# Optimization experiments

Measured on AMD Instinct MI355X. Metric: run time of the kernel, lower is better.

Reference implementation:

```python
import jax, jax.numpy as jnp
import numpy as np

N_NODES = 100000
BN_EPS = 1e-5


def gcn_conv(x, W, b, src, dst, n_nodes):
    # PyG GCNConv: linear transform, add self loops, symmetric deg^-1/2 normalization, sum-aggregate to dst, add bias
    h = x @ W.T  # [N, out_dim]
    loops = jnp.arange(n_nodes, dtype=src.dtype)
    src_a = jnp.concatenate([src, loops])
    dst_a = jnp.concatenate([dst, loops])
    deg = jnp.zeros((n_nodes,), dtype=h.dtype).at[dst_a].add(1.0)  # includes self loops, so deg >= 1
    dinv = jax.lax.rsqrt(deg)
    norm = dinv[src_a] * dinv[dst_a]  # [E+N]
    msgs = h[src_a] * norm[:, None]  # gather + scale
    out = jax.ops.segment_sum(msgs, dst_a, num_segments=n_nodes)
    return out + b


def batch_norm(x, gamma, beta):
    # BatchNorm1d in training mode: per-feature batch mean/var (biased)
    mean = jnp.mean(x, axis=0)
    var = jnp.var(x, axis=0)
    return (x - mean) * jax.lax.rsqrt(var + BN_EPS) * gamma + beta


def setup_inputs() -> dict:
    key = jax.random.key(0)
    ks = jax.random.split(key, 8)
    n, e = N_NODES, 1600000
    d_in, d_hid, d_out = 128, 128, 64
    x = jax.random.normal(ks[0], (n, d_in), dtype=jnp.float32)
    edge_index = jax.random.randint(ks[1], (2, e), 0, n, dtype=jnp.int64)
    W1 = jax.random.normal(ks[2], (d_hid, d_in), dtype=jnp.float32) / np.sqrt(d_in)
    b1 = jnp.zeros((d_hid,), dtype=jnp.float32)
    gamma = jnp.ones((d_hid,), dtype=jnp.float32)
    beta = jnp.zeros((d_hid,), dtype=jnp.float32)
    W2 = jax.random.normal(ks[3], (d_out, d_hid), dtype=jnp.float32) / np.sqrt(d_hid)
    b2 = jnp.zeros((d_out,), dtype=jnp.float32)
    return {"x": x, "edge_index": edge_index, "W1": W1, "b1": b1,
            "gamma": gamma, "beta": beta, "W2": W2, "b2": b2}


def reference(x, edge_index, W1, b1, gamma, beta, W2, b2):
    src, dst = edge_index[0], edge_index[1]
    n = x.shape[0]
    h = gcn_conv(x, W1, b1, src, dst, n)          # layer 0 conv
    h = batch_norm(h, gamma, beta)                 # BN
    h = jax.nn.relu(h)                             # ReLU (dropout p=0 -> identity)
    out = gcn_conv(h, W2, b2, src, dst, n)         # layer 1 conv (no BN/act on last layer)
    return out
```

## Files before the change

### kernel.cpp

```cpp
#include <hip/hip_runtime.h>

constexpr float BN_EPS = 1e-5f;
#define BSH 7
#define NBMAX 1024

typedef __attribute__((ext_vector_type(8))) short bf16x8;
typedef __attribute__((ext_vector_type(4))) float f32x4;

__device__ inline float2 bf2x2(unsigned int v) {
    union { unsigned int i; float f; } a, b;
    a.i = v << 16;
    b.i = v & 0xFFFF0000u;
    return make_float2(a.f, b.f);
}
__device__ inline float bf2f(unsigned short u) {
    union { unsigned int i; float f; } a;
    a.i = ((unsigned int)u) << 16;
    return a.f;
}
__device__ inline unsigned short f2bf(float f) {
    union { float f; unsigned int i; } c;
    c.f = f;
    unsigned int i = c.i;
    return (unsigned short)((i + 0x7FFFu + ((i >> 16) & 1u)) >> 16);
}

__device__ inline int wsw(int row, int k) {
    return row * 128 + ((((k >> 3) ^ (row & 7)) << 3) | (k & 7));
}

__global__ void k_zero(int* __restrict__ gcount) {
    gcount[threadIdx.x] = 0;
}

__global__ __launch_bounds__(256) void k_hist(const int* __restrict__ dst, int* __restrict__ gcount,
                                              int E, int NB) {
    __shared__ int lh[NBMAX];
    const int tid = threadIdx.x;
    for (int i = tid; i < NBMAX; i += 256) lh[i] = 0;
    __syncthreads();
    const int base = blockIdx.x * 8192;
#pragma unroll
    for (int i = 0; i < 32; ++i) {
        int e = base + i * 256 + tid;
        if (e < E) atomicAdd(&lh[dst[e] >> BSH], 1);
    }
    __syncthreads();
    for (int b = tid; b < NB; b += 256) {
        int c = lh[b];
        if (c) atomicAdd(&gcount[b], c);
    }
}

__global__ __launch_bounds__(1024) void k_scanb(const int* __restrict__ gcount, int* __restrict__ gstart,
                                                int* __restrict__ cursor, float* __restrict__ stats, int NB) {
    __shared__ int tmp[1024];
    const int t = threadIdx.x;
    int v = (t < NB) ? gcount[t] : 0;
    tmp[t] = v;
    __syncthreads();
    for (int off = 1; off < 1024; off <<= 1) {
        int u = (t >= off) ? tmp[t - off] : 0;
        __syncthreads();
        tmp[t] += u;
        __syncthreads();
    }
    if (t < NB) { int ex = tmp[t] - v; gstart[t] = ex; cursor[t] = ex; }
    if (t == NB - 1) gstart[NB] = tmp[t];
    if (t < 512) stats[t] = 0.f;
}

__global__ __launch_bounds__(256) void k_scatter(const int* __restrict__ src, const int* __restrict__ dst,
                                                 int* __restrict__ cursor, int2* __restrict__ pairs,
                                                 int E, int NB) {
    __shared__ int lh[NBMAX], lbase[NBMAX], gbase[NBMAX], lcur[NBMAX];
    __shared__ int2 buf[4096];
    __shared__ unsigned short bo[4096];
    const int tid = threadIdx.x;
    for (int i = tid; i < NBMAX; i += 256) lh[i] = 0;
    __syncthreads();
    const int base = blockIdx.x * 4096;
    const int cnt = min(4096, E - base);
#pragma unroll
    for (int i = 0; i < 16; ++i) {
        int e = base + i * 256 + tid;
        if (e < E) atomicAdd(&lh[dst[e] >> BSH], 1);
    }
    __syncthreads();
    int s0 = lh[tid * 4], s1 = lh[tid * 4 + 1], s2 = lh[tid * 4 + 2], s3 = lh[tid * 4 + 3];
    int ts = s0 + s1 + s2 + s3;
    lcur[tid] = ts;
    __syncthreads();
    for (int off = 1; off < 256; off <<= 1) {
        int u = (tid >= off) ? lcur[tid - off] : 0;
        __syncthreads();
        lcur[tid] += u;
        __syncthreads();
    }
    int ex = lcur[tid] - ts;
    lbase[tid * 4] = ex;
    lbase[tid * 4 + 1] = ex + s0;
    lbase[tid * 4 + 2] = ex + s0 + s1;
    lbase[tid * 4 + 3] = ex + s0 + s1 + s2;
    __syncthreads();
    for (int b = tid; b < NB; b += 256) {
        int c = lh[b];
        gbase[b] = c ? atomicAdd(&cursor[b], c) : 0;
    }
    for (int i = tid; i < NBMAX; i += 256) lcur[i] = 0;
    __syncthreads();
#pragma unroll
    for (int i = 0; i < 16; ++i) {
        int e = base + i * 256 + tid;
        if (e < E) {
            int d = dst[e];
            int b = d >> BSH;
            int p = lbase[b] + atomicAdd(&lcur[b], 1);
            buf[p] = make_int2(src[e], d);
            bo[p] = (unsigned short)b;
        }
    }
    __syncthreads();
#pragma unroll
    for (int i = 0; i < 16; ++i) {
        int p = i * 256 + tid;
        if (p < cnt) {
            int b = bo[p];
            pairs[gbase[b] + (p - lbase[b])] = buf[p];
        }
    }
}

__global__ __launch_bounds__(256) void k_build(const int2* __restrict__ pairs, const int* __restrict__ gstart,
                                               int* __restrict__ rowptr, int* __restrict__ rowend,
                                               float* __restrict__ dinv, int* __restrict__ esrc, int n) {
    __shared__ int lh[128], lsc[128], lcur[128];
    const int tid = threadIdx.x;
    const int b = blockIdx.x;
    const int e0 = gstart[b], e1 = gstart[b + 1];
    const int node0 = b << BSH;
    if (tid < 128) lh[tid] = 0;
    __syncthreads();
    for (int e = e0 + tid; e < e1; e += 256) atomicAdd(&lh[pairs[e].y - node0], 1);
    __syncthreads();
    int v = (tid < 128) ? lh[tid] : 0;
    if (tid < 128) lsc[tid] = v;
    __syncthreads();
    for (int off = 1; off < 128; off <<= 1) {
        int u = (tid >= off && tid < 128) ? lsc[tid - off] : 0;
        __syncthreads();
        if (tid < 128) lsc[tid] += u;
        __syncthreads();
    }
    if (tid < 128) {
        int ex = lsc[tid] - v;
        lcur[tid] = ex;
        int node = node0 + tid;
        if (node < n) {
            int rp = e0 + ex;
            rowptr[node] = rp;
            rowend[node] = rp + v;
            dinv[node] = rsqrtf((float)(v + 1));
        }
    }
    __syncthreads();
    for (int e = e0 + tid; e < e1; e += 256) {
        int2 p = pairs[e];
        int pos = atomicAdd(&lcur[p.y - node0], 1);
        esrc[e0 + pos] = p.x;
    }
}

__global__ __launch_bounds__(256) void k_gemm1(const float* __restrict__ x,
                                               const float* __restrict__ W1,
                                               const float* __restrict__ dinv,
                                               unsigned short* __restrict__ g1, int n) {
    __shared__ unsigned short Ws[128 * 128];
    const int tid = threadIdx.x;
#pragma unroll
    for (int i = 0; i < 16; ++i) {
        int idx4 = i * 256 + tid;
        int j = idx4 >> 5;
        int k = (idx4 & 31) * 4;
        float4 v = *(const float4*)&W1[(size_t)j * 128 + k];
        ushort4 u;
        u.x = f2bf(v.x); u.y = f2bf(v.y); u.z = f2bf(v.z); u.w = f2bf(v.w);
        *(ushort2*)&Ws[wsw(j, k)] = make_ushort2(u.x, u.y);
        *(ushort2*)&Ws[wsw(j, k + 2)] = make_ushort2(u.z, u.w);
    }
    __syncthreads();
    const int wave = tid >> 6, l = tid & 63;
    const int am = l & 15;
    const int kg = l >> 4;
    const int row0 = blockIdx.x * 64 + wave * 16;
    const int grow = row0 + am;
    const float* xrow = &x[(size_t)(grow < n ? grow : 0) * 128];
    f32x4 acc[8] = {};
#pragma unroll
    for (int k0 = 0; k0 < 128; k0 += 32) {
        const int kk = k0 + kg * 8;
        float4 a0 = *(const float4*)&xrow[kk];
        float4 a1 = *(const float4*)&xrow[kk + 4];
        union { unsigned short u[8]; bf16x8 v; } af;
        af.u[0] = f2bf(a0.x); af.u[1] = f2bf(a0.y); af.u[2] = f2bf(a0.z); af.u[3] = f2bf(a0.w);
        af.u[4] = f2bf(a1.x); af.u[5] = f2bf(a1.y); af.u[6] = f2bf(a1.z); af.u[7] = f2bf(a1.w);
#pragma unroll
        for (int ct = 0; ct < 8; ++ct) {
            union { uint4 q; bf16x8 v; } bf;
            bf.q = *(const uint4*)&Ws[wsw(ct * 16 + am, kk)];
            acc[ct] = __builtin_amdgcn_mfma_f32_16x16x32_bf16(af.v, bf.v, acc[ct], 0, 0, 0);
        }
    }
#pragma unroll
    for (int r = 0; r < 4; ++r) {
        int orow = row0 + kg * 4 + r;
        if (orow < n) {
            float di = dinv[orow];
#pragma unroll
            for (int ct = 0; ct < 8; ++ct)
                g1[(size_t)orow * 128 + ct * 16 + am] = f2bf(acc[ct][r] * di);
        }
    }
}

__global__ __launch_bounds__(256) void k_pull1(const int* __restrict__ rowptr, const int* __restrict__ rowend,
                                               const int* __restrict__ esrc, const unsigned short* __restrict__ g,
                                               const float* __restrict__ dinv, const float* __restrict__ b1,
                                               unsigned short* __restrict__ h1, float* __restrict__ stats, int n) {
    __shared__ float2 sSum[4][64];
    __shared__ float2 sSq[4][64];
    const int wid = threadIdx.x >> 6, lane = threadIdx.x & 63;
    const int gw = blockIdx.x * 4 + wid;
    const int nw = gridDim.x * 4;
    const float2 bias = *(const float2*)&b1[lane * 2];
    float2 psum = {0.f, 0.f}, psq = {0.f, 0.f};
    for (int node = gw; node < n; node += nw) {
        const int b = rowptr[node], e = rowend[node];
        float2 a0 = bf2x2(*(const unsigned int*)&g[(size_t)node * 128 + lane * 2]);
        float2 a1 = {0.f, 0.f}, a2 = {0.f, 0.f}, a3 = {0.f, 0.f};
        float2 a4 = {0.f, 0.f}, a5 = {0.f, 0.f}, a6 = {0.f, 0.f}, a7 = {0.f, 0.f};
        int j = b;
        for (; j + 8 <= e; j += 8) {
            int s0 = esrc[j + 0], s1 = esrc[j + 1], s2 = esrc[j + 2], s3 = esrc[j + 3];
            int s4 = esrc[j + 4], s5 = esrc[j + 5], s6 = esrc[j + 6], s7 = esrc[j + 7];
            unsigned int v0 = *(const unsigned int*)&g[(size_t)s0 * 128 + lane * 2];
            unsigned int v1 = *(const unsigned int*)&g[(size_t)s1 * 128 + lane * 2];
            unsigned int v2 = *(const unsigned int*)&g[(size_t)s2 * 128 + lane * 2];
            unsigned int v3 = *(const unsigned int*)&g[(size_t)s3 * 128 + lane * 2];
            unsigned int v4 = *(const unsigned int*)&g[(size_t)s4 * 128 + lane * 2];
            unsigned int v5 = *(const unsigned int*)&g[(size_t)s5 * 128 + lane * 2];
            unsigned int v6 = *(const unsigned int*)&g[(size_t)s6 * 128 + lane * 2];
            unsigned int v7 = *(const unsigned int*)&g[(size_t)s7 * 128 + lane * 2];
            float2 f0 = bf2x2(v0), f1 = bf2x2(v1), f2 = bf2x2(v2), f3 = bf2x2(v3);
            float2 f4 = bf2x2(v4), f5 = bf2x2(v5), f6 = bf2x2(v6), f7 = bf2x2(v7);
            a0.x += f0.x; a0.y += f0.y;
            a1.x += f1.x; a1.y += f1.y;
            a2.x += f2.x; a2.y += f2.y;
            a3.x += f3.x; a3.y += f3.y;
            a4.x += f4.x; a4.y += f4.y;
            a5.x += f5.x; a5.y += f5.y;
            a6.x += f6.x; a6.y += f6.y;
            a7.x += f7.x; a7.y += f7.y;
        }
        for (; j < e; ++j) {
            int s = esrc[j];
            float2 v = bf2x2(*(const unsigned int*)&g[(size_t)s * 128 + lane * 2]);
            a0.x += v.x; a0.y += v.y;
        }
        float2 acc = {((a0.x + a1.x) + (a2.x + a3.x)) + ((a4.x + a5.x) + (a6.x + a7.x)),
                      ((a0.y + a1.y) + (a2.y + a3.y)) + ((a4.y + a5.y) + (a6.y + a7.y))};
        const float di = dinv[node];
        float2 hv = {fmaf(acc.x, di, bias.x), fmaf(acc.y, di, bias.y)};
        unsigned int pk = ((unsigned int)f2bf(hv.y) << 16) | (unsigned int)f2bf(hv.x);
        *(unsigned int*)&h1[(size_t)node * 128 + lane * 2] = pk;
        psum.x += hv.x; psum.y += hv.y;
        psq.x = fmaf(hv.x, hv.x, psq.x);
        psq.y = fmaf(hv.y, hv.y, psq.y);
    }
    sSum[wid][lane] = psum;
    sSq[wid][lane] = psq;
    __syncthreads();
    if (threadIdx.x < 64) {
        float2 a = sSum[0][lane], b = sSum[1][lane], c = sSum[2][lane], d = sSum[3][lane];
        atomicAdd(&stats[lane * 2 + 0], a.x + b.x + c.x + d.x);
        atomicAdd(&stats[lane * 2 + 1], a.y + b.y + c.y + d.y);
        a = sSq[0][lane]; b = sSq[1][lane]; c = sSq[2][lane]; d = sSq[3][lane];
        atomicAdd(&stats[128 + lane * 2 + 0], a.x + b.x + c.x + d.x);
        atomicAdd(&stats[128 + lane * 2 + 1], a.y + b.y + c.y + d.y);
    }
}

__global__ void k_bnfinal(float* __restrict__ stats, const float* __restrict__ gamma,
                          const float* __restrict__ beta, int n) {
    int f = threadIdx.x;
    float inv_n = 1.f / (float)n;
    float mean = stats[f] * inv_n;
    float var = stats[128 + f] * inv_n - mean * mean;
    float sc = gamma[f] * rsqrtf(var + BN_EPS);
    stats[256 + f] = sc;
    stats[384 + f] = fmaf(-mean, sc, beta[f]);
}

__global__ __launch_bounds__(256) void k_gemm2(const unsigned short* __restrict__ h1,
                                               const float* __restrict__ W2,
                                               const float* __restrict__ dinv,
                                               const float* __restrict__ stats,
                                               unsigned short* __restrict__ g2, int n) {
    __shared__ unsigned short Ws[64 * 128];
    const int tid = threadIdx.x;
#pragma unroll
    for (int i = 0; i < 8; ++i) {
        int idx4 = i * 256 + tid;
        int j = idx4 >> 5;
        int k = (idx4 & 31) * 4;
        float4 v = *(const float4*)&W2[(size_t)j * 128 + k];
        ushort4 u;
        u.x = f2bf(v.x); u.y = f2bf(v.y); u.z = f2bf(v.z); u.w = f2bf(v.w);
        *(ushort2*)&Ws[wsw(j, k)] = make_ushort2(u.x, u.y);
        *(ushort2*)&Ws[wsw(j, k + 2)] = make_ushort2(u.z, u.w);
    }
    __syncthreads();
    const int wave = tid >> 6, l = tid & 63;
    const int am = l & 15;
    const int kg = l >> 4;
    const int row0 = blockIdx.x * 64 + wave * 16;
    const int grow = row0 + am;
    const unsigned short* hrow = &h1[(size_t)(grow < n ? grow : 0) * 128];
    f32x4 acc[4] = {};
#pragma unroll
    for (int k0 = 0; k0 < 128; k0 += 32) {
        const int kk = k0 + kg * 8;
        uint4 hq = *(const uint4*)&hrow[kk];
        float2 p0 = bf2x2(hq.x), p1 = bf2x2(hq.y), p2 = bf2x2(hq.z), p3 = bf2x2(hq.w);
        float hf[8] = {p0.x, p0.y, p1.x, p1.y, p2.x, p2.y, p3.x, p3.y};
        float4 sc0 = *(const float4*)&stats[256 + kk];
        float4 sc1 = *(const float4*)&stats[256 + kk + 4];
        float4 sh0 = *(const float4*)&stats[384 + kk];
        float4 sh1 = *(const float4*)&stats[384 + kk + 4];
        float scv[8] = {sc0.x, sc0.y, sc0.z, sc0.w, sc1.x, sc1.y, sc1.z, sc1.w};
        float shv[8] = {sh0.x, sh0.y, sh0.z, sh0.w, sh1.x, sh1.y, sh1.z, sh1.w};
        union { unsigned short u[8]; bf16x8 v; } af;
#pragma unroll
        for (int jj = 0; jj < 8; ++jj)
            af.u[jj] = f2bf(fmaxf(fmaf(hf[jj], scv[jj], shv[jj]), 0.f));
#pragma unroll
        for (int ct = 0; ct < 4; ++ct) {
            union { uint4 q; bf16x8 v; } bf;
            bf.q = *(const uint4*)&Ws[wsw(ct * 16 + am, kk)];
            acc[ct] = __builtin_amdgcn_mfma_f32_16x16x32_bf16(af.v, bf.v, acc[ct], 0, 0, 0);
        }
    }
#pragma unroll
    for (int r = 0; r < 4; ++r) {
        int orow = row0 + kg * 4 + r;
        if (orow < n) {
            float di = dinv[orow];
#pragma unroll
            for (int ct = 0; ct < 4; ++ct)
                g2[(size_t)orow * 64 + ct * 16 + am] = f2bf(acc[ct][r] * di);
        }
    }
}

__global__ __launch_bounds__(256) void k_pull2(const int* __restrict__ rowptr, const int* __restrict__ rowend,
                                               const int* __restrict__ esrc, const unsigned short* __restrict__ g,
                                               const float* __restrict__ dinv, const float* __restrict__ b2,
                                               float* __restrict__ out, int n) {
    const int wid = threadIdx.x >> 6, lane = threadIdx.x & 63;
    const int gw = blockIdx.x * 4 + wid;
    const int nw = gridDim.x * 4;
    const float bias = b2[lane];
    for (int node = gw; node < n; node += nw) {
        const int b = rowptr[node], e = rowend[node];
        float a0 = bf2f(g[(size_t)node * 64 + lane]);
        float a1 = 0.f, a2 = 0.f, a3 = 0.f, a4 = 0.f, a5 = 0.f, a6 = 0.f, a7 = 0.f;
        int j = b;
        for (; j + 8 <= e; j += 8) {
            int s0 = esrc[j + 0], s1 = esrc[j + 1], s2 = esrc[j + 2], s3 = esrc[j + 3];
            int s4 = esrc[j + 4], s5 = esrc[j + 5], s6 = esrc[j + 6], s7 = esrc[j + 7];
            unsigned short v0 = g[(size_t)s0 * 64 + lane];
            unsigned short v1 = g[(size_t)s1 * 64 + lane];
            unsigned short v2 = g[(size_t)s2 * 64 + lane];
            unsigned short v3 = g[(size_t)s3 * 64 + lane];
            unsigned short v4 = g[(size_t)s4 * 64 + lane];
            unsigned short v5 = g[(size_t)s5 * 64 + lane];
            unsigned short v6 = g[(size_t)s6 * 64 + lane];
            unsigned short v7 = g[(size_t)s7 * 64 + lane];
            a0 += bf2f(v0); a1 += bf2f(v1); a2 += bf2f(v2); a3 += bf2f(v3);
            a4 += bf2f(v4); a5 += bf2f(v5); a6 += bf2f(v6); a7 += bf2f(v7);
        }
        for (; j < e; ++j) a0 += bf2f(g[(size_t)esrc[j] * 64 + lane]);
        float acc = ((a0 + a1) + (a2 + a3)) + ((a4 + a5) + (a6 + a7));
        out[(size_t)node * 64 + lane] = fmaf(acc, dinv[node], bias);
    }
}

extern "C" void kernel_launch(void* const* d_in, const int* in_sizes, int n_in,
                              void* d_out, int out_size, void* d_ws, size_t ws_size,
                              hipStream_t stream) {
    const float* x     = (const float*)d_in[0];
    const int*   ei    = (const int*)d_in[1];
    const float* W1    = (const float*)d_in[2];
    const float* b1    = (const float*)d_in[3];
    const float* gamma = (const float*)d_in[4];
    const float* beta  = (const float*)d_in[5];
    const float* W2    = (const float*)d_in[6];
    const float* b2    = (const float*)d_in[7];
    float* out = (float*)d_out;

    const int n = in_sizes[0] / 128;
    const int E = in_sizes[1] / 2;
    const int* src = ei;
    const int* dst = ei + E;
    const int NB = (n + 127) >> BSH;
    const int Np = (n + 255) & ~255;
    const int Ep = (E + 3) & ~3;

    char* ws = (char*)d_ws;
    int*   gcount = (int*)ws;
    int*   gstart = gcount + 1024;
    int*   cursor = gstart + 1088;
    float* stats  = (float*)(cursor + 1024);
    float* dinv   = stats + 512;
    int*   rowptr = (int*)(dinv + Np);
    int*   rowend = rowptr + Np;
    int2*  pairs  = (int2*)(rowend + Np);
    int*   esrc   = (int*)(pairs + Ep);
    unsigned short* g1 = (unsigned short*)(esrc + Ep);
    unsigned short* h1 = g1 + (size_t)n * 128;
    unsigned short* g2 = g1;

    const int gb = (n + 63) / 64;
    const int gh = (E + 8191) / 8192;
    const int gs = (E + 4095) / 4096;

    hipLaunchKernelGGL(k_zero, dim3(1), dim3(1024), 0, stream, gcount);
    hipLaunchKernelGGL(k_hist, dim3(gh), dim3(256), 0, stream, dst, gcount, E, NB);
    hipLaunchKernelGGL(k_scanb, dim3(1), dim3(1024), 0, stream, gcount, gstart, cursor, stats, NB);
    hipLaunchKernelGGL(k_scatter, dim3(gs), dim3(256), 0, stream, src, dst, cursor, pairs, E, NB);
    hipLaunchKernelGGL(k_build, dim3(NB), dim3(256), 0, stream, pairs, gstart, rowptr, rowend, dinv, esrc, n);

    hipLaunchKernelGGL(k_gemm1, dim3(gb), dim3(256), 0, stream, x, W1, dinv, g1, n);
    hipLaunchKernelGGL(k_pull1, dim3(2048), dim3(256), 0, stream, rowptr, rowend, esrc, g1, dinv, b1, h1, stats, n);
    hipLaunchKernelGGL(k_bnfinal, dim3(1), dim3(128), 0, stream, stats, gamma, beta, n);

    hipLaunchKernelGGL(k_gemm2, dim3(gb), dim3(256), 0, stream, h1, W2, dinv, stats, g2, n);
    hipLaunchKernelGGL(k_pull2, dim3(2048), dim3(256), 0, stream, rowptr, rowend, esrc, g2, dinv, b2, out, n);
}
```

Before: 319.6 us.

## Pack edge pairs into one int, add nontemporal hints, fold BN finalize into gemm2

Edge pairs are packed into a single 32-bit word (20-bit source, 7-bit local dst offset), which halves the scatter/build intermediate traffic and the shared buffer size. Streaming loads and stores of dst, esrc, h1 and out now use nontemporal hints so they do not pollute the cache used for the gathered features. The separate BN finalize kernel is removed, and each gemm2 block recomputes scale and shift into shared memory, saving one launch at the cost of redundant per-block work. Packing assumes node ids fit in 20 bits (n up to about 1M).

```diff
diff --git a/kernel.cpp b/kernel.cpp
--- a/kernel.cpp
+++ b/kernel.cpp
@@ -43,7 +43,7 @@
 #pragma unroll
     for (int i = 0; i < 32; ++i) {
         int e = base + i * 256 + tid;
-        if (e < E) atomicAdd(&lh[dst[e] >> BSH], 1);
+        if (e < E) atomicAdd(&lh[__builtin_nontemporal_load(&dst[e]) >> BSH], 1);
     }
     __syncthreads();
     for (int b = tid; b < NB; b += 256) {
@@ -71,10 +71,10 @@
 }
 
 __global__ __launch_bounds__(256) void k_scatter(const int* __restrict__ src, const int* __restrict__ dst,
-                                                 int* __restrict__ cursor, int2* __restrict__ pairs,
+                                                 int* __restrict__ cursor, int* __restrict__ pairs,
                                                  int E, int NB) {
     __shared__ int lh[NBMAX], lbase[NBMAX], gbase[NBMAX], lcur[NBMAX];
-    __shared__ int2 buf[4096];
+    __shared__ int buf[4096];
     __shared__ unsigned short bo[4096];
     const int tid = threadIdx.x;
     for (int i = tid; i < NBMAX; i += 256) lh[i] = 0;
@@ -84,7 +84,7 @@
 #pragma unroll
     for (int i = 0; i < 16; ++i) {
         int e = base + i * 256 + tid;
-        if (e < E) atomicAdd(&lh[dst[e] >> BSH], 1);
+        if (e < E) atomicAdd(&lh[__builtin_nontemporal_load(&dst[e]) >> BSH], 1);
     }
     __syncthreads();
     int s0 = lh[tid * 4], s1 = lh[tid * 4 + 1], s2 = lh[tid * 4 + 2], s3 = lh[tid * 4 + 3];
@@ -116,7 +116,7 @@
             int d = dst[e];
             int b = d >> BSH;
             int p = lbase[b] + atomicAdd(&lcur[b], 1);
-            buf[p] = make_int2(src[e], d);
+            buf[p] = src[e] | ((d & ((1 << BSH) - 1)) << 20);
             bo[p] = (unsigned short)b;
         }
     }
@@ -126,12 +126,12 @@
         int p = i * 256 + tid;
         if (p < cnt) {
             int b = bo[p];
-            pairs[gbase[b] + (p - lbase[b])] = buf[p];
-        }
-    }
-}
-
-__global__ __launch_bounds__(256) void k_build(const int2* __restrict__ pairs, const int* __restrict__ gstart,
+            __builtin_nontemporal_store(buf[p], &pairs[gbase[b] + (p - lbase[b])]);
+        }
+    }
+}
+
+__global__ __launch_bounds__(256) void k_build(const int* __restrict__ pairs, const int* __restrict__ gstart,
                                                int* __restrict__ rowptr, int* __restrict__ rowend,
                                                float* __restrict__ dinv, int* __restrict__ esrc, int n) {
     __shared__ int lh[128], lsc[128], lcur[128];
@@ -141,7 +141,7 @@
     const int node0 = b << BSH;
     if (tid < 128) lh[tid] = 0;
     __syncthreads();
-    for (int e = e0 + tid; e < e1; e += 256) atomicAdd(&lh[pairs[e].y - node0], 1);
+    for (int e = e0 + tid; e < e1; e += 256) atomicAdd(&lh[pairs[e] >> 20], 1);
     __syncthreads();
     int v = (tid < 128) ? lh[tid] : 0;
     if (tid < 128) lsc[tid] = v;
@@ -165,9 +165,9 @@
     }
     __syncthreads();
     for (int e = e0 + tid; e < e1; e += 256) {
-        int2 p = pairs[e];
-        int pos = atomicAdd(&lcur[p.y - node0], 1);
-        esrc[e0 + pos] = p.x;
+        int pv = pairs[e];
+        int pos = atomicAdd(&lcur[pv >> 20], 1);
+        __builtin_nontemporal_store(pv & 0xFFFFF, &esrc[e0 + pos]);
     }
 }
 
@@ -241,8 +241,14 @@
         float2 a4 = {0.f, 0.f}, a5 = {0.f, 0.f}, a6 = {0.f, 0.f}, a7 = {0.f, 0.f};
         int j = b;
         for (; j + 8 <= e; j += 8) {
-            int s0 = esrc[j + 0], s1 = esrc[j + 1], s2 = esrc[j + 2], s3 = esrc[j + 3];
-            int s4 = esrc[j + 4], s5 = esrc[j + 5], s6 = esrc[j + 6], s7 = esrc[j + 7];
+            int s0 = __builtin_nontemporal_load(&esrc[j + 0]);
+            int s1 = __builtin_nontemporal_load(&esrc[j + 1]);
+            int s2 = __builtin_nontemporal_load(&esrc[j + 2]);
+            int s3 = __builtin_nontemporal_load(&esrc[j + 3]);
+            int s4 = __builtin_nontemporal_load(&esrc[j + 4]);
+            int s5 = __builtin_nontemporal_load(&esrc[j + 5]);
+            int s6 = __builtin_nontemporal_load(&esrc[j + 6]);
+            int s7 = __builtin_nontemporal_load(&esrc[j + 7]);
             unsigned int v0 = *(const unsigned int*)&g[(size_t)s0 * 128 + lane * 2];
             unsigned int v1 = *(const unsigned int*)&g[(size_t)s1 * 128 + lane * 2];
             unsigned int v2 = *(const unsigned int*)&g[(size_t)s2 * 128 + lane * 2];
@@ -263,7 +269,7 @@
             a7.x += f7.x; a7.y += f7.y;
         }
         for (; j < e; ++j) {
-            int s = esrc[j];
+            int s = __builtin_nontemporal_load(&esrc[j]);
             float2 v = bf2x2(*(const unsigned int*)&g[(size_t)s * 128 + lane * 2]);
             a0.x += v.x; a0.y += v.y;
         }
@@ -272,7 +278,7 @@
         const float di = dinv[node];
         float2 hv = {fmaf(acc.x, di, bias.x), fmaf(acc.y, di, bias.y)};
         unsigned int pk = ((unsigned int)f2bf(hv.y) << 16) | (unsigned int)f2bf(hv.x);
-        *(unsigned int*)&h1[(size_t)node * 128 + lane * 2] = pk;
+        __builtin_nontemporal_store(pk, (unsigned int*)&h1[(size_t)node * 128 + lane * 2]);
         psum.x += hv.x; psum.y += hv.y;
         psq.x = fmaf(hv.x, hv.x, psq.x);
         psq.y = fmaf(hv.y, hv.y, psq.y);
@@ -290,24 +296,24 @@
     }
 }
 
-__global__ void k_bnfinal(float* __restrict__ stats, const float* __restrict__ gamma,
-                          const float* __restrict__ beta, int n) {
-    int f = threadIdx.x;
-    float inv_n = 1.f / (float)n;
-    float mean = stats[f] * inv_n;
-    float var = stats[128 + f] * inv_n - mean * mean;
-    float sc = gamma[f] * rsqrtf(var + BN_EPS);
-    stats[256 + f] = sc;
-    stats[384 + f] = fmaf(-mean, sc, beta[f]);
-}
-
 __global__ __launch_bounds__(256) void k_gemm2(const unsigned short* __restrict__ h1,
                                                const float* __restrict__ W2,
                                                const float* __restrict__ dinv,
                                                const float* __restrict__ stats,
+                                               const float* __restrict__ gamma,
+                                               const float* __restrict__ beta,
                                                unsigned short* __restrict__ g2, int n) {
     __shared__ unsigned short Ws[64 * 128];
+    __shared__ float sSc[128], sSh[128];
     const int tid = threadIdx.x;
+    if (tid < 128) {
+        float inv_n = 1.f / (float)n;
+        float mean = stats[tid] * inv_n;
+        float var = stats[128 + tid] * inv_n - mean * mean;
+        float sc = gamma[tid] * rsqrtf(var + BN_EPS);
+        sSc[tid] = sc;
+        sSh[tid] = fmaf(-mean, sc, beta[tid]);
+    }
 #pragma unroll
     for (int i = 0; i < 8; ++i) {
         int idx4 = i * 256 + tid;
@@ -333,10 +339,10 @@
         uint4 hq = *(const uint4*)&hrow[kk];
         float2 p0 = bf2x2(hq.x), p1 = bf2x2(hq.y), p2 = bf2x2(hq.z), p3 = bf2x2(hq.w);
         float hf[8] = {p0.x, p0.y, p1.x, p1.y, p2.x, p2.y, p3.x, p3.y};
-        float4 sc0 = *(const float4*)&stats[256 + kk];
-        float4 sc1 = *(const float4*)&stats[256 + kk + 4];
-        float4 sh0 = *(const float4*)&stats[384 + kk];
-        float4 sh1 = *(const float4*)&stats[384 + kk + 4];
+        float4 sc0 = *(const float4*)&sSc[kk];
+        float4 sc1 = *(const float4*)&sSc[kk + 4];
+        float4 sh0 = *(const float4*)&sSh[kk];
+        float4 sh1 = *(const float4*)&sSh[kk + 4];
         float scv[8] = {sc0.x, sc0.y, sc0.z, sc0.w, sc1.x, sc1.y, sc1.z, sc1.w};
         float shv[8] = {sh0.x, sh0.y, sh0.z, sh0.w, sh1.x, sh1.y, sh1.z, sh1.w};
         union { unsigned short u[8]; bf16x8 v; } af;
@@ -376,8 +382,14 @@
         float a1 = 0.f, a2 = 0.f, a3 = 0.f, a4 = 0.f, a5 = 0.f, a6 = 0.f, a7 = 0.f;
         int j = b;
         for (; j + 8 <= e; j += 8) {
-            int s0 = esrc[j + 0], s1 = esrc[j + 1], s2 = esrc[j + 2], s3 = esrc[j + 3];
-            int s4 = esrc[j + 4], s5 = esrc[j + 5], s6 = esrc[j + 6], s7 = esrc[j + 7];
+            int s0 = __builtin_nontemporal_load(&esrc[j + 0]);
+            int s1 = __builtin_nontemporal_load(&esrc[j + 1]);
+            int s2 = __builtin_nontemporal_load(&esrc[j + 2]);
+            int s3 = __builtin_nontemporal_load(&esrc[j + 3]);
+            int s4 = __builtin_nontemporal_load(&esrc[j + 4]);
+            int s5 = __builtin_nontemporal_load(&esrc[j + 5]);
+            int s6 = __builtin_nontemporal_load(&esrc[j + 6]);
+            int s7 = __builtin_nontemporal_load(&esrc[j + 7]);
             unsigned short v0 = g[(size_t)s0 * 64 + lane];
             unsigned short v1 = g[(size_t)s1 * 64 + lane];
             unsigned short v2 = g[(size_t)s2 * 64 + lane];
@@ -389,9 +401,9 @@
             a0 += bf2f(v0); a1 += bf2f(v1); a2 += bf2f(v2); a3 += bf2f(v3);
             a4 += bf2f(v4); a5 += bf2f(v5); a6 += bf2f(v6); a7 += bf2f(v7);
         }
-        for (; j < e; ++j) a0 += bf2f(g[(size_t)esrc[j] * 64 + lane]);
+        for (; j < e; ++j) a0 += bf2f(g[(size_t)__builtin_nontemporal_load(&esrc[j]) * 64 + lane]);
         float acc = ((a0 + a1) + (a2 + a3)) + ((a4 + a5) + (a6 + a7));
-        out[(size_t)node * 64 + lane] = fmaf(acc, dinv[node], bias);
+        __builtin_nontemporal_store(fmaf(acc, dinv[node], bias), &out[(size_t)node * 64 + lane]);
     }
 }
 
@@ -424,8 +436,8 @@
     float* dinv   = stats + 512;
     int*   rowptr = (int*)(dinv + Np);
     int*   rowend = rowptr + Np;
-    int2*  pairs  = (int2*)(rowend + Np);
-    int*   esrc   = (int*)(pairs + Ep);
+    int*   pairs  = rowend + Np;
+    int*   esrc   = pairs + Ep;
     unsigned short* g1 = (unsigned short*)(esrc + Ep);
     unsigned short* h1 = g1 + (size_t)n * 128;
     unsigned short* g2 = g1;
@@ -442,8 +454,7 @@
 
     hipLaunchKernelGGL(k_gemm1, dim3(gb), dim3(256), 0, stream, x, W1, dinv, g1, n);
     hipLaunchKernelGGL(k_pull1, dim3(2048), dim3(256), 0, stream, rowptr, rowend, esrc, g1, dinv, b1, h1, stats, n);
-    hipLaunchKernelGGL(k_bnfinal, dim3(1), dim3(128), 0, stream, stats, gamma, beta, n);
-
-    hipLaunchKernelGGL(k_gemm2, dim3(gb), dim3(256), 0, stream, h1, W2, dinv, stats, g2, n);
+
+    hipLaunchKernelGGL(k_gemm2, dim3(gb), dim3(256), 0, stream, h1, W2, dinv, stats, gamma, beta, g2, n);
     hipLaunchKernelGGL(k_pull2, dim3(2048), dim3(256), 0, stream, rowptr, rowend, esrc, g2, dinv, b2, out, n);
 }
```

After: 384.5 us. 20.3% more time.
